# Optimization experiments

Hardware: AMD Instinct MI355X
Metric: run time of the kernel (lower is better)

Reference implementation:

```python
import jax, jax.numpy as jnp
import numpy as np

H = 16  # num_heads

def setup_inputs() -> dict:
    key = jax.random.key(0)
    ks = jax.random.split(key, 6)
    B, N, D = 2, 2048, 1024
    s = 0.02
    return {
        "x": jax.random.normal(ks[0], (B, N, D), jnp.float32),
        "attn_bias": jax.random.normal(ks[1], (B, N), jnp.float32),
        "w_qkv": jax.random.normal(ks[2], (D, 3 * D), jnp.float32) * s,
        "b_qkv": jnp.zeros((3 * D,), jnp.float32),
        "w_proj": jax.random.normal(ks[3], (D, D), jnp.float32) * s,
        "b_proj": jnp.zeros((D,), jnp.float32),
    }

def reference(x, attn_bias, w_qkv, b_qkv, w_proj, b_proj):
    B, N, D = x.shape
    hd = D // H
    qkv = x @ w_qkv + b_qkv                       # (B,N,3D)
    qkv = qkv.reshape(B, N, 3, H, hd)
    q, k, v = qkv[:, :, 0], qkv[:, :, 1], qkv[:, :, 2]  # (B,N,H,hd)
    scores = jnp.einsum("bqhd,bkhd->bhqk", q, k) / np.sqrt(hd).astype(x.dtype)
    scores = scores + attn_bias[:, None, None, :]  # key-wise bias (B,1,1,N)
    w = jax.nn.softmax(scores, axis=-1)
    out = jnp.einsum("bhqk,bkhd->bqhd", w, v).reshape(B, N, D)
    return out @ w_proj + b_proj
```

## Files before the change

### kernel.cpp

```cpp
#include <hip/hip_runtime.h>
#include <stdint.h>

typedef __attribute__((ext_vector_type(8))) short bf16x8;
typedef __attribute__((ext_vector_type(4))) short s16x4;
typedef __attribute__((ext_vector_type(4))) float f32x4;
typedef __attribute__((ext_vector_type(4))) unsigned int u32x4;

#define DEV __device__ __forceinline__

DEV unsigned short f2bf(float f) {
    unsigned u = __builtin_bit_cast(unsigned, f);
    u += 0x7FFFu + ((u >> 16) & 1u);
    return (unsigned short)(u >> 16);
}

DEV void gload_lds16(const void* g, void* l) {
    __builtin_amdgcn_global_load_lds(
        (const __attribute__((address_space(1))) unsigned int*)g,
        (__attribute__((address_space(3))) unsigned int*)l,
        16, 0, 0);
}

__global__ __launch_bounds__(256) void cvt_f32_bf16(
    const float* __restrict__ in, unsigned short* __restrict__ out, int n4) {
    int i = blockIdx.x * blockDim.x + threadIdx.x;
    if (i >= n4) return;
    const float4 v = reinterpret_cast<const float4*>(in)[i];
    s16x4 o;
    o.x = (short)f2bf(v.x); o.y = (short)f2bf(v.y);
    o.z = (short)f2bf(v.z); o.w = (short)f2bf(v.w);
    reinterpret_cast<s16x4*>(out)[i] = o;
}

__global__ __launch_bounds__(256) void transpose_w(
    const float* __restrict__ w, unsigned short* __restrict__ wt, int K, int N) {
    __shared__ unsigned short tile[64][72];
    const int k0 = blockIdx.y * 64, n0 = blockIdx.x * 64;
    const int t = threadIdx.x;
    #pragma unroll
    for (int i = 0; i < 4; ++i) {
        const int e = t + i * 256;
        const int r = e >> 4, c4 = e & 15;
        const float4 v = *reinterpret_cast<const float4*>(w + (size_t)(k0 + r) * N + n0 + c4 * 4);
        s16x4 o;
        o.x = (short)f2bf(v.x); o.y = (short)f2bf(v.y);
        o.z = (short)f2bf(v.z); o.w = (short)f2bf(v.w);
        *(s16x4*)&tile[r][c4 * 4] = o;
    }
    __syncthreads();
    #pragma unroll
    for (int i = 0; i < 4; ++i) {
        const int e = t + i * 256;
        const int rn = e >> 4, c4 = e & 15;
        s16x4 o;
        o.x = (short)tile[c4 * 4 + 0][rn];
        o.y = (short)tile[c4 * 4 + 1][rn];
        o.z = (short)tile[c4 * 4 + 2][rn];
        o.w = (short)tile[c4 * 4 + 3][rn];
        *(s16x4*)(wt + (size_t)(n0 + rn) * K + k0 + c4 * 4) = o;
    }
}

__global__ __launch_bounds__(512, 2)
void gemm256_qkv(const unsigned short* __restrict__ A,
                 const unsigned short* __restrict__ BT,
                 const float* __restrict__ bias,
                 unsigned short* __restrict__ q_out,
                 unsigned short* __restrict__ k_out,
                 unsigned short* __restrict__ v_out)
{
    constexpr int K = 1024;
    constexpr int NT = 16;
    __shared__ unsigned short lds[2][2][2][2][128][32];

    const int t = threadIdx.x;
    const int wave = t >> 6, lane = t & 63;
    const int l15 = lane & 15, l4 = lane >> 4;
    const int wr = wave >> 2, wc = wave & 3;

    const int lin = blockIdx.x;
    const int logical = (lin & 7) * 24 + (lin >> 3);
    const int bx = logical % 12, by = logical / 12;
    const int tile_m = by * 256, tile_n = bx * 256;

    const int st_row = t >> 2;
    const int st_col = ((t & 3) ^ ((t >> 3) & 3)) * 8;
    const int cswz   = (l4 ^ ((l15 >> 1) & 3)) * 8;

    f32x4 acc[8][4] = {};
    bf16x8 ra[4], rb[4];

    #define STAGE(buf, ab, half, kk, k0)                                           \
        gload_lds16(((ab) ? BT : A) +                                              \
                        (size_t)(((ab) ? tile_n : tile_m) + (half) * 128 + st_row) * K \
                        + (k0) + (kk) * 32 + st_col,                               \
                    &lds[buf][ab][half][kk][0][0] + wave * 512)
    #define READ_A(buf, kk, mq)                                                    \
        _Pragma("unroll") for (int i = 0; i < 4; ++i)                              \
            ra[i] = *(const bf16x8*)&lds[buf][0][wr][kk][((mq) * 4 + i) * 16 + l15][cswz];
    #define READ_B(buf, kk)                                                        \
        _Pragma("unroll") for (int n = 0; n < 4; ++n)                              \
            rb[n] = *(const bf16x8*)&lds[buf][1][wc >> 1][kk][(wc & 1) * 64 + n * 16 + l15][cswz];
    #define MFMA16(mq)                                                             \
        __builtin_amdgcn_s_setprio(1);                                             \
        _Pragma("unroll") for (int i = 0; i < 4; ++i)                              \
            _Pragma("unroll") for (int n = 0; n < 4; ++n)                          \
                acc[(mq) * 4 + i][n] = __builtin_amdgcn_mfma_f32_16x16x32_bf16(    \
                    ra[i], rb[n], acc[(mq) * 4 + i][n], 0, 0, 0);                  \
        __builtin_amdgcn_s_setprio(0);
    #define BAR()   __builtin_amdgcn_s_barrier()
    #define LGKM0() do { asm volatile("s_waitcnt lgkmcnt(0)" ::: "memory");        \
                         __builtin_amdgcn_sched_barrier(0); } while (0)

    STAGE(0, 1, 0, 0, 0);  STAGE(0, 1, 1, 0, 0);
    STAGE(0, 0, 0, 0, 0);  STAGE(0, 0, 1, 0, 0);
    STAGE(0, 1, 0, 1, 0);  STAGE(0, 1, 1, 1, 0);
    STAGE(0, 0, 0, 1, 0);  STAGE(0, 0, 1, 1, 0);
    STAGE(1, 1, 0, 0, 64); STAGE(1, 1, 1, 0, 64);
    STAGE(1, 0, 0, 0, 64); STAGE(1, 0, 1, 0, 64);
    STAGE(1, 1, 0, 1, 64); STAGE(1, 1, 1, 1, 64);
    asm volatile("s_waitcnt vmcnt(6)" ::: "memory");
    BAR();

    for (int kt = 0; kt < NT; ++kt) {
        const int buf = kt & 1;
        const int k0 = kt * 64;
        const bool s1 = (kt + 1 < NT);
        const bool s234 = (kt + 2 < NT);

        READ_A(buf, 0, 0); READ_B(buf, 0);
        if (s1) { STAGE(buf ^ 1, 0, 0, 1, k0 + 64); STAGE(buf ^ 1, 0, 1, 1, k0 + 64); }
        BAR(); LGKM0();
        MFMA16(0);
        BAR();

        READ_A(buf, 0, 1);
        if (s234) { STAGE(buf, 1, 0, 0, k0 + 128); STAGE(buf, 1, 1, 0, k0 + 128); }
        BAR(); LGKM0();
        MFMA16(1);
        BAR();

        READ_A(buf, 1, 0); READ_B(buf, 1);
        if (s234) { STAGE(buf, 0, 0, 0, k0 + 128); STAGE(buf, 0, 1, 0, k0 + 128); }
        BAR(); LGKM0();
        MFMA16(0);
        BAR();

        READ_A(buf, 1, 1);
        if (s234) { STAGE(buf, 1, 0, 1, k0 + 128); STAGE(buf, 1, 1, 1, k0 + 128); }
        BAR(); LGKM0();
        MFMA16(1);
        if (kt < NT - 2)       asm volatile("s_waitcnt vmcnt(6)" ::: "memory");
        else if (kt == NT - 2) asm volatile("s_waitcnt vmcnt(0)" ::: "memory");
        if (kt < NT - 1) BAR();
    }
    #undef STAGE
    #undef READ_A
    #undef READ_B
    #undef MFMA16
    #undef BAR
    #undef LGKM0

    float bcol[4];
    #pragma unroll
    for (int n = 0; n < 4; ++n) bcol[n] = bias[tile_n + wc * 64 + n * 16 + l15];

    #pragma unroll
    for (int m = 0; m < 8; ++m)
        #pragma unroll
        for (int n = 0; n < 4; ++n) {
            const int col = tile_n + wc * 64 + n * 16 + l15;
            const int which = col >> 10;
            const int hh = (col >> 6) & 15;
            const int d = col & 63;
            const int row0 = tile_m + wr * 128 + m * 16 + l4 * 4;
            const int bb = row0 >> 11, nn = row0 & 2047;
            if (which == 2) {
                const int nl = nn & 63;
                const int np = (nl & 32) | ((nl & 12) << 1) | ((nl & 16) >> 2) | (nl & 3);
                const size_t dstV = ((size_t)((bb * 16 + hh) * 64 + d)) * 2048 + (nn & ~63) + np;
                s16x4 pk;
                #pragma unroll
                for (int r = 0; r < 4; ++r) pk[r] = (short)f2bf(acc[m][n][r] + bcol[n]);
                *(s16x4*)&v_out[dstV] = pk;
            } else {
                #pragma unroll
                for (int r = 0; r < 4; ++r) {
                    const float v = acc[m][n][r] + bcol[n];
                    const size_t dst = ((size_t)((bb * 16 + hh) * 2048 + nn + r)) * 64 + d;
                    if (which == 0) q_out[dst] = f2bf(v * 0.125f);
                    else            k_out[dst] = f2bf(v);
                }
            }
        }
}

__global__ __launch_bounds__(256)
void gemm_bf16_f32out(const unsigned short* __restrict__ A,
                      const unsigned short* __restrict__ BT,
                      const float* __restrict__ bias,
                      float* __restrict__ f_out,
                      int M, int N, int K)
{
    __shared__ unsigned short Abuf[128 * 64];
    __shared__ unsigned short Bbuf[128 * 64];

    const int t = threadIdx.x;
    const int wave = t >> 6, lane = t & 63;
    const int l15 = lane & 15, l4 = lane >> 4;
    const int wr = wave >> 1, wc = wave & 1;
    const int tile_m = blockIdx.y * 128, tile_n = blockIdx.x * 128;

    const int srow = wave * 32 + (lane >> 3);
    const int scol = (lane & 7) * 8;

    f32x4 acc[4][4] = {};

    const int nk = K >> 6;
    for (int kt = 0; kt < nk; ++kt) {
        const int k0 = kt << 6;
        __syncthreads();
        #pragma unroll
        for (int c = 0; c < 4; ++c) {
            const unsigned short* sa = A + (size_t)(tile_m + srow + c * 8) * K + k0 + scol;
            gload_lds16(sa, &Abuf[(wave * 32 + c * 8) * 64]);
            const unsigned short* sb = BT + (size_t)(tile_n + srow + c * 8) * K + k0 + scol;
            gload_lds16(sb, &Bbuf[(wave * 32 + c * 8) * 64]);
        }
        asm volatile("s_waitcnt vmcnt(0)" ::: "memory");
        __syncthreads();

        bf16x8 ra[4][2], rb[4][2];
        #pragma unroll
        for (int m = 0; m < 4; ++m)
            #pragma unroll
            for (int ks = 0; ks < 2; ++ks)
                ra[m][ks] = *(const bf16x8*)&Abuf[(wr * 64 + m * 16 + l15) * 64 + ks * 32 + l4 * 8];
        #pragma unroll
        for (int n = 0; n < 4; ++n)
            #pragma unroll
            for (int ks = 0; ks < 2; ++ks)
                rb[n][ks] = *(const bf16x8*)&Bbuf[(wc * 64 + n * 16 + l15) * 64 + ks * 32 + l4 * 8];

        #pragma unroll
        for (int m = 0; m < 4; ++m)
            #pragma unroll
            for (int n = 0; n < 4; ++n) {
                acc[m][n] = __builtin_amdgcn_mfma_f32_16x16x32_bf16(ra[m][0], rb[n][0], acc[m][n], 0, 0, 0);
                acc[m][n] = __builtin_amdgcn_mfma_f32_16x16x32_bf16(ra[m][1], rb[n][1], acc[m][n], 0, 0, 0);
            }
    }

    float bcol[4];
    #pragma unroll
    for (int n = 0; n < 4; ++n) bcol[n] = bias[tile_n + wc * 64 + n * 16 + l15];

    #pragma unroll
    for (int m = 0; m < 4; ++m)
        #pragma unroll
        for (int n = 0; n < 4; ++n) {
            const int col = tile_n + wc * 64 + n * 16 + l15;
            #pragma unroll
            for (int r = 0; r < 4; ++r) {
                const int row = tile_m + wr * 64 + m * 16 + l4 * 4 + r;
                f_out[(size_t)row * N + col] = acc[m][n][r] + bcol[n];
            }
        }
}

__global__ __launch_bounds__(512, 4)
void attn_kernel(const unsigned short* __restrict__ Qb,
                 const unsigned short* __restrict__ Kb,
                 const unsigned short* __restrict__ Vt,
                 const float* __restrict__ bias,
                 unsigned short* __restrict__ Ob)
{
    __shared__ __align__(16) unsigned char pool[40960];
    unsigned short (*Kf)[4096] = (unsigned short (*)[4096])(pool);
    unsigned short (*Vf)[4096] = (unsigned short (*)[4096])(pool + 16384);
    float* blds = (float*)(pool + 32768);
    float (*Oscr)[32][64] = (float (*)[32][64])(pool);
    float (*Lscr)[4][32]  = (float (*)[4][32])(pool + 32768);

    const unsigned di = blockIdx.x;
    const unsigned logical = (di & 7) * 64 + (di >> 3);
    const int qt = logical & 15;
    const int h  = (logical >> 4) & 15;
    const int b  = logical >> 8;

    const int t = threadIdx.x;
    const int wave = t >> 6, lane = t & 63;
    const int l15 = lane & 15, l4 = lane >> 4;
    const int wq = wave & 3, wk = wave >> 2;
    const int kb0 = wk * 32;
    const int xsw = (l15 & 7) << 3;

    const size_t head = ((size_t)(b * 16 + h)) * 2048 * 64;
    const unsigned short* Qh = Qb + head;
    const unsigned short* Kh = Kb + head;

    const int srow8 = wave * 8 + (lane >> 3);
    const int scol8 = 8 * ((lane & 7) ^ (lane >> 3));
    const unsigned short* Ksrc = Kh + (size_t)srow8 * 64 + scol8;
    const unsigned short* Vsrc = Vt + ((size_t)((b * 16 + h) * 64) + srow8) * 2048 + scol8;

    for (int i = t; i < 2048; i += 512) blds[i] = bias[b * 2048 + i] - 5.5451774f;

    const int qbase = qt * 128 + wq * 32;
    bf16x8 qf[2][2];
    #pragma unroll
    for (int qi = 0; qi < 2; ++qi)
        #pragma unroll
        for (int ks = 0; ks < 2; ++ks)
            qf[qi][ks] = *(const bf16x8*)(Qh + (size_t)(qbase + qi * 16 + l15) * 64 + ks * 32 + l4 * 8);

    float lsum[2] = {0.f, 0.f};
    f32x4 oacc[2][4] = {};

    gload_lds16(Ksrc, &Kf[0][wave * 512]);
    gload_lds16(Vsrc, &Vf[0][wave * 512]);
    __syncthreads();

    for (int kt = 0; kt < 32; ++kt) {
        const int key0 = kt * 64;
        const int pb = kt & 1;

        if (kt < 31) {
            gload_lds16(Ksrc + (size_t)(key0 + 64) * 64, &Kf[pb ^ 1][wave * 512]);
            gload_lds16(Vsrc + key0 + 64, &Vf[pb ^ 1][wave * 512]);
        }

        const unsigned short* Kp = Kf[pb];
        const unsigned short* Vp = Vf[pb];

        bf16x8 kfr[2][2];
        #pragma unroll
        for (int f = 0; f < 2; ++f)
            #pragma unroll
            for (int ks = 0; ks < 2; ++ks)
                kfr[f][ks] = *(const bf16x8*)&Kp[(kb0 + f * 16 + l15) * 64 + ((ks * 32 + l4 * 8) ^ xsw)];

        f32x4 bk[2];
        #pragma unroll
        for (int f = 0; f < 2; ++f)
            bk[f] = *(const f32x4*)&blds[key0 + kb0 + f * 16 + l4 * 4];

        f32x4 s[2][2];
        __builtin_amdgcn_s_setprio(1);
        #pragma unroll
        for (int qi = 0; qi < 2; ++qi)
            #pragma unroll
            for (int f = 0; f < 2; ++f) {
                f32x4 z = bk[f];
                z = __builtin_amdgcn_mfma_f32_16x16x32_bf16(kfr[f][0], qf[qi][0], z, 0, 0, 0);
                z = __builtin_amdgcn_mfma_f32_16x16x32_bf16(kfr[f][1], qf[qi][1], z, 0, 0, 0);
                s[qi][f] = z;
            }
        __builtin_amdgcn_s_setprio(0);

        bf16x8 pa[2];
        #pragma unroll
        for (int qi = 0; qi < 2; ++qi) {
            float ps = 0.f;
            u32x4 w;
            #pragma unroll
            for (int f = 0; f < 2; ++f) {
                const float p0 = __expf(s[qi][f][0]);
                const float p1 = __expf(s[qi][f][1]);
                const float p2 = __expf(s[qi][f][2]);
                const float p3 = __expf(s[qi][f][3]);
                ps += (p0 + p1) + (p2 + p3);
                unsigned w0, w1;
                asm("v_cvt_pk_bf16_f32 %0, %1, %2" : "=v"(w0) : "v"(p0), "v"(p1));
                asm("v_cvt_pk_bf16_f32 %0, %1, %2" : "=v"(w1) : "v"(p2), "v"(p3));
                w[f * 2] = w0; w[f * 2 + 1] = w1;
            }
            lsum[qi] += ps;
            pa[qi] = __builtin_bit_cast(bf16x8, w);
        }

        __builtin_amdgcn_s_setprio(1);
        #pragma unroll
        for (int df = 0; df < 4; ++df) {
            bf16x8 vf = *(const bf16x8*)&Vp[(df * 16 + l15) * 64 + ((kb0 + l4 * 8) ^ xsw)];
            oacc[0][df] = __builtin_amdgcn_mfma_f32_16x16x32_bf16(pa[0], vf, oacc[0][df], 0, 0, 0);
            oacc[1][df] = __builtin_amdgcn_mfma_f32_16x16x32_bf16(pa[1], vf, oacc[1][df], 0, 0, 0);
        }
        __builtin_amdgcn_s_setprio(0);

        __syncthreads();
    }

    #pragma unroll
    for (int qi = 0; qi < 2; ++qi) {
        lsum[qi] += __shfl_xor(lsum[qi], 16, 64);
        lsum[qi] += __shfl_xor(lsum[qi], 32, 64);
    }

    __syncthreads();
    if (lane < 16) {
        Lscr[wk][wq][lane] = lsum[0];
        Lscr[wk][wq][16 + lane] = lsum[1];
    }
    if (wk == 1) {
        #pragma unroll
        for (int qi = 0; qi < 2; ++qi)
            #pragma unroll
            for (int df = 0; df < 4; ++df)
                #pragma unroll
                for (int r = 0; r < 4; ++r)
                    Oscr[wq][qi * 16 + l4 * 4 + r][df * 16 + l15] = oacc[qi][df][r];
    }
    __syncthreads();
    if (wk == 0) {
        #pragma unroll
        for (int qi = 0; qi < 2; ++qi) {
            float inv[4];
            #pragma unroll
            for (int r = 0; r < 4; ++r) {
                const int ql = qi * 16 + l4 * 4 + r;
                inv[r] = 1.0f / (Lscr[0][wq][ql] + Lscr[1][wq][ql]);
            }
            #pragma unroll
            for (int r = 0; r < 4; ++r) {
                const int ql = qi * 16 + l4 * 4 + r;
                const int q = qbase + ql;
                #pragma unroll
                for (int df = 0; df < 4; ++df) {
                    const int d = df * 16 + l15;
                    const float v = oacc[qi][df][r] + Oscr[wq][ql][d];
                    Ob[((size_t)(b * 2048 + q)) * 1024 + h * 64 + d] = f2bf(v * inv[r]);
                }
            }
        }
    }
}

extern "C" void kernel_launch(void* const* d_in, const int* in_sizes, int n_in,
                              void* d_out, int out_size, void* d_ws, size_t ws_size,
                              hipStream_t stream) {
    const float* x      = (const float*)d_in[0];
    const float* abias  = (const float*)d_in[1];
    const float* w_qkv  = (const float*)d_in[2];
    const float* b_qkv  = (const float*)d_in[3];
    const float* w_proj = (const float*)d_in[4];
    const float* b_proj = (const float*)d_in[5];
    float* out = (float*)d_out;

    unsigned short* ws = (unsigned short*)d_ws;
    unsigned short* xb  = ws;
    unsigned short* wqT = xb  + (size_t)4096 * 1024;
    unsigned short* wpT = wqT + (size_t)3072 * 1024;
    unsigned short* qb  = wpT + (size_t)1024 * 1024;
    unsigned short* kb  = qb  + (size_t)2 * 16 * 2048 * 64;
    unsigned short* vt  = kb  + (size_t)2 * 16 * 2048 * 64;
    unsigned short* ao  = vt  + (size_t)2 * 16 * 2048 * 64;

    cvt_f32_bf16<<<4096, 256, 0, stream>>>(x, xb, 1048576);
    transpose_w<<<dim3(48, 16), 256, 0, stream>>>(w_qkv, wqT, 1024, 3072);
    transpose_w<<<dim3(16, 16), 256, 0, stream>>>(w_proj, wpT, 1024, 1024);
    gemm256_qkv<<<192, 512, 0, stream>>>(xb, wqT, b_qkv, qb, kb, vt);
    attn_kernel<<<512, 512, 0, stream>>>(qb, kb, vt, abias, ao);
    gemm_bf16_f32out<<<dim3(8, 32), 256, 0, stream>>>(ao, wpT, b_proj, out, 4096, 1024, 1024);
}
```

Measured before the change: 120.3 us.

## Double attention block to 1024 threads with one 16-row query tile per wave

The attention kernel now launches 1024 threads per block, and each wave handles 16 query rows instead of 32, so work is spread over 16 waves. K and V tile loads are split by wave: the first 8 waves fetch K and the last 8 fetch V. This is meant to raise wave-level parallelism and latency hiding while cutting per-wave register use. In exchange, each K fragment read from LDS is reused across fewer query rows, and more waves synchronise at every barrier.

```diff
diff --git a/kernel.cpp b/kernel.cpp
--- a/kernel.cpp
+++ b/kernel.cpp
@@ -268,7 +268,7 @@
         }
 }
 
-__global__ __launch_bounds__(512, 4)
+__global__ __launch_bounds__(1024, 8)
 void attn_kernel(const unsigned short* __restrict__ Qb,
                  const unsigned short* __restrict__ Kb,
                  const unsigned short* __restrict__ Vt,
@@ -279,8 +279,8 @@
     unsigned short (*Kf)[4096] = (unsigned short (*)[4096])(pool);
     unsigned short (*Vf)[4096] = (unsigned short (*)[4096])(pool + 16384);
     float* blds = (float*)(pool + 32768);
-    float (*Oscr)[32][64] = (float (*)[32][64])(pool);
-    float (*Lscr)[4][32]  = (float (*)[4][32])(pool + 32768);
+    float (*Oscr)[16][64] = (float (*)[16][64])(pool);
+    float (*Lscr)[8][16]  = (float (*)[8][16])(pool + 32768);
 
     const unsigned di = blockIdx.x;
     const unsigned logical = (di & 7) * 64 + (di >> 3);
@@ -291,7 +291,7 @@
     const int t = threadIdx.x;
     const int wave = t >> 6, lane = t & 63;
     const int l15 = lane & 15, l4 = lane >> 4;
-    const int wq = wave & 3, wk = wave >> 2;
+    const int wq = wave >> 1, wk = wave & 1;
     const int kb0 = wk * 32;
     const int xsw = (l15 & 7) << 3;
 
@@ -299,36 +299,36 @@
     const unsigned short* Qh = Qb + head;
     const unsigned short* Kh = Kb + head;
 
-    const int srow8 = wave * 8 + (lane >> 3);
+    const int w8 = wave & 7;
+    const int srow8 = w8 * 8 + (lane >> 3);
     const int scol8 = 8 * ((lane & 7) ^ (lane >> 3));
-    const unsigned short* Ksrc = Kh + (size_t)srow8 * 64 + scol8;
-    const unsigned short* Vsrc = Vt + ((size_t)((b * 16 + h) * 64) + srow8) * 2048 + scol8;
-
-    for (int i = t; i < 2048; i += 512) blds[i] = bias[b * 2048 + i] - 5.5451774f;
-
-    const int qbase = qt * 128 + wq * 32;
-    bf16x8 qf[2][2];
-    #pragma unroll
-    for (int qi = 0; qi < 2; ++qi)
-        #pragma unroll
-        for (int ks = 0; ks < 2; ++ks)
-            qf[qi][ks] = *(const bf16x8*)(Qh + (size_t)(qbase + qi * 16 + l15) * 64 + ks * 32 + l4 * 8);
-
-    float lsum[2] = {0.f, 0.f};
-    f32x4 oacc[2][4] = {};
-
-    gload_lds16(Ksrc, &Kf[0][wave * 512]);
-    gload_lds16(Vsrc, &Vf[0][wave * 512]);
+    const unsigned short* Src = (wave < 8)
+        ? Kh + (size_t)srow8 * 64 + scol8
+        : Vt + ((size_t)((b * 16 + h) * 64) + srow8) * 2048 + scol8;
+    const int sstep = (wave < 8) ? 64 * 64 : 64;
+    unsigned short* ldst_base0 = (wave < 8) ? &Kf[0][w8 * 512] : &Vf[0][w8 * 512];
+    unsigned short* ldst_base1 = (wave < 8) ? &Kf[1][w8 * 512] : &Vf[1][w8 * 512];
+
+    for (int i = t; i < 2048; i += 1024) blds[i] = bias[b * 2048 + i] - 5.5451774f;
+
+    const int qbase = qt * 128 + wq * 16;
+    bf16x8 qf[2];
+    #pragma unroll
+    for (int ks = 0; ks < 2; ++ks)
+        qf[ks] = *(const bf16x8*)(Qh + (size_t)(qbase + l15) * 64 + ks * 32 + l4 * 8);
+
+    float lsum = 0.f;
+    f32x4 oacc[4] = {};
+
+    gload_lds16(Src, ldst_base0);
     __syncthreads();
 
     for (int kt = 0; kt < 32; ++kt) {
         const int key0 = kt * 64;
         const int pb = kt & 1;
 
-        if (kt < 31) {
-            gload_lds16(Ksrc + (size_t)(key0 + 64) * 64, &Kf[pb ^ 1][wave * 512]);
-            gload_lds16(Vsrc + key0 + 64, &Vf[pb ^ 1][wave * 512]);
-        }
+        if (kt < 31)
+            gload_lds16(Src + (size_t)(kt + 1) * sstep, pb ? ldst_base0 : ldst_base1);
 
         const unsigned short* Kp = Kf[pb];
         const unsigned short* Vp = Vf[pb];
@@ -345,92 +345,74 @@
         for (int f = 0; f < 2; ++f)
             bk[f] = *(const f32x4*)&blds[key0 + kb0 + f * 16 + l4 * 4];
 
-        f32x4 s[2][2];
+        f32x4 s[2];
         __builtin_amdgcn_s_setprio(1);
         #pragma unroll
-        for (int qi = 0; qi < 2; ++qi)
-            #pragma unroll
-            for (int f = 0; f < 2; ++f) {
-                f32x4 z = bk[f];
-                z = __builtin_amdgcn_mfma_f32_16x16x32_bf16(kfr[f][0], qf[qi][0], z, 0, 0, 0);
-                z = __builtin_amdgcn_mfma_f32_16x16x32_bf16(kfr[f][1], qf[qi][1], z, 0, 0, 0);
-                s[qi][f] = z;
-            }
+        for (int f = 0; f < 2; ++f) {
+            f32x4 z = bk[f];
+            z = __builtin_amdgcn_mfma_f32_16x16x32_bf16(kfr[f][0], qf[0], z, 0, 0, 0);
+            z = __builtin_amdgcn_mfma_f32_16x16x32_bf16(kfr[f][1], qf[1], z, 0, 0, 0);
+            s[f] = z;
+        }
         __builtin_amdgcn_s_setprio(0);
 
-        bf16x8 pa[2];
-        #pragma unroll
-        for (int qi = 0; qi < 2; ++qi) {
-            float ps = 0.f;
-            u32x4 w;
-            #pragma unroll
-            for (int f = 0; f < 2; ++f) {
-                const float p0 = __expf(s[qi][f][0]);
-                const float p1 = __expf(s[qi][f][1]);
-                const float p2 = __expf(s[qi][f][2]);
-                const float p3 = __expf(s[qi][f][3]);
-                ps += (p0 + p1) + (p2 + p3);
-                unsigned w0, w1;
-                asm("v_cvt_pk_bf16_f32 %0, %1, %2" : "=v"(w0) : "v"(p0), "v"(p1));
-                asm("v_cvt_pk_bf16_f32 %0, %1, %2" : "=v"(w1) : "v"(p2), "v"(p3));
-                w[f * 2] = w0; w[f * 2 + 1] = w1;
-            }
-            lsum[qi] += ps;
-            pa[qi] = __builtin_bit_cast(bf16x8, w);
-        }
+        float ps = 0.f;
+        u32x4 w;
+        #pragma unroll
+        for (int f = 0; f < 2; ++f) {
+            const float p0 = __expf(s[f][0]);
+            const float p1 = __expf(s[f][1]);
+            const float p2 = __expf(s[f][2]);
+            const float p3 = __expf(s[f][3]);
+            ps += (p0 + p1) + (p2 + p3);
+            unsigned w0, w1;
+            asm("v_cvt_pk_bf16_f32 %0, %1, %2" : "=v"(w0) : "v"(p0), "v"(p1));
+            asm("v_cvt_pk_bf16_f32 %0, %1, %2" : "=v"(w1) : "v"(p2), "v"(p3));
+            w[f * 2] = w0; w[f * 2 + 1] = w1;
+        }
+        lsum += ps;
+        const bf16x8 pa = __builtin_bit_cast(bf16x8, w);
 
         __builtin_amdgcn_s_setprio(1);
         #pragma unroll
         for (int df = 0; df < 4; ++df) {
             bf16x8 vf = *(const bf16x8*)&Vp[(df * 16 + l15) * 64 + ((kb0 + l4 * 8) ^ xsw)];
-            oacc[0][df] = __builtin_amdgcn_mfma_f32_16x16x32_bf16(pa[0], vf, oacc[0][df], 0, 0, 0);
-            oacc[1][df] = __builtin_amdgcn_mfma_f32_16x16x32_bf16(pa[1], vf, oacc[1][df], 0, 0, 0);
+            oacc[df] = __builtin_amdgcn_mfma_f32_16x16x32_bf16(pa, vf, oacc[df], 0, 0, 0);
         }
         __builtin_amdgcn_s_setprio(0);
 
         __syncthreads();
     }
 
-    #pragma unroll
-    for (int qi = 0; qi < 2; ++qi) {
-        lsum[qi] += __shfl_xor(lsum[qi], 16, 64);
-        lsum[qi] += __shfl_xor(lsum[qi], 32, 64);
-    }
+    lsum += __shfl_xor(lsum, 16, 64);
+    lsum += __shfl_xor(lsum, 32, 64);
 
     __syncthreads();
-    if (lane < 16) {
-        Lscr[wk][wq][lane] = lsum[0];
-        Lscr[wk][wq][16 + lane] = lsum[1];
-    }
+    if (lane < 16) Lscr[wk][wq][lane] = lsum;
     if (wk == 1) {
         #pragma unroll
-        for (int qi = 0; qi < 2; ++qi)
-            #pragma unroll
-            for (int df = 0; df < 4; ++df)
-                #pragma unroll
-                for (int r = 0; r < 4; ++r)
-                    Oscr[wq][qi * 16 + l4 * 4 + r][df * 16 + l15] = oacc[qi][df][r];
+        for (int df = 0; df < 4; ++df)
+            #pragma unroll
+            for (int r = 0; r < 4; ++r)
+                Oscr[wq][l4 * 4 + r][df * 16 + l15] = oacc[df][r];
     }
     __syncthreads();
     if (wk == 0) {
-        #pragma unroll
-        for (int qi = 0; qi < 2; ++qi) {
-            float inv[4];
-            #pragma unroll
-            for (int r = 0; r < 4; ++r) {
-                const int ql = qi * 16 + l4 * 4 + r;
-                inv[r] = 1.0f / (Lscr[0][wq][ql] + Lscr[1][wq][ql]);
-            }
-            #pragma unroll
-            for (int r = 0; r < 4; ++r) {
-                const int ql = qi * 16 + l4 * 4 + r;
-                const int q = qbase + ql;
-                #pragma unroll
-                for (int df = 0; df < 4; ++df) {
-                    const int d = df * 16 + l15;
-                    const float v = oacc[qi][df][r] + Oscr[wq][ql][d];
-                    Ob[((size_t)(b * 2048 + q)) * 1024 + h * 64 + d] = f2bf(v * inv[r]);
-                }
+        float inv[4];
+        #pragma unroll
+        for (int r = 0; r < 4; ++r) {
+            const int ql = l4 * 4 + r;
+            inv[r] = 1.0f / (Lscr[0][wq][ql] + Lscr[1][wq][ql]);
+        }
+        #pragma unroll
+        for (int r = 0; r < 4; ++r) {
+            const int ql = l4 * 4 + r;
+            const int q = qbase + ql;
+            #pragma unroll
+            for (int df = 0; df < 4; ++df) {
+                const int d = df * 16 + l15;
+                const float v = oacc[df][r] + Oscr[wq][ql][d];
+                Ob[((size_t)(b * 2048 + q)) * 1024 + h * 64 + d] = f2bf(v * inv[r]);
             }
         }
     }
@@ -460,6 +442,6 @@
     transpose_w<<<dim3(48, 16), 256, 0, stream>>>(w_qkv, wqT, 1024, 3072);
     transpose_w<<<dim3(16, 16), 256, 0, stream>>>(w_proj, wpT, 1024, 1024);
     gemm256_qkv<<<192, 512, 0, stream>>>(xb, wqT, b_qkv, qb, kb, vt);
-    attn_kernel<<<512, 512, 0, stream>>>(qb, kb, vt, abias, ao);
+    attn_kernel<<<512, 1024, 0, stream>>>(qb, kb, vt, abias, ao);
     gemm_bf16_f32out<<<dim3(8, 32), 256, 0, stream>>>(ao, wpT, b_proj, out, 4096, 1024, 1024);
 }
```

After: 124.7 us. 1.04x slower.
